# Performance work log

Measured on AMD Instinct MI355X. Metric: run time of the kernel, lower is better.

Reference implementation:

```python
import jax, jax.numpy as jnp
import numpy as np

RADIUS = 0.1
NSAMPLE = 32


def setup_inputs() -> dict:
    key = jax.random.key(0)
    k1, k2, k3, k4 = jax.random.split(key, 4)
    B, N, C = 8, 8192, 64
    C_in = 3 + C  # relative xyz concatenated with features
    H1, H2 = 64, 128
    xyz = jax.random.uniform(k1, (B, N, 3), dtype=jnp.float32)  # points in unit cube
    features = jax.random.normal(k2, (B, C, N), dtype=jnp.float32)
    W1 = jax.random.normal(k3, (H1, C_in), dtype=jnp.float32) / np.sqrt(C_in)
    b1 = jnp.zeros((H1,), dtype=jnp.float32)
    W2 = jax.random.normal(k4, (H2, H1), dtype=jnp.float32) / np.sqrt(H1)
    b2 = jnp.zeros((H2,), dtype=jnp.float32)
    return {"xyz": xyz, "features": features, "W1": W1, "b1": b1,
            "W2": W2, "b2": b2, "npoint": 2048}


def _ball_query(xyz, new_xyz, radius, nsample):
    # xyz: (B,N,3), new_xyz: (B,S,3) -> idx (B,S,nsample) int32
    N = xyz.shape[1]
    d2 = jnp.sum((new_xyz[:, :, None, :] - xyz[:, None, :, :]) ** 2, axis=-1)  # (B,S,N)
    mask = d2 < radius * radius
    # sort key: in-ball points keep their index (ascending order first),
    # out-of-ball points pushed behind by +N
    ar = jnp.arange(N, dtype=jnp.int32)
    key = jnp.where(mask, ar, ar + N)
    idx_sorted = jnp.argsort(key, axis=-1)[..., :nsample].astype(jnp.int32)  # (B,S,ns)
    count = jnp.sum(mask, axis=-1)  # (B,S)
    first = idx_sorted[..., :1]
    slot = jnp.arange(nsample)
    # CUDA ball_query pads missing slots with the first found index
    return jnp.where(slot[None, None, :] < count[..., None], idx_sorted, first)


def reference(xyz, features, W1, b1, W2, b2, npoint):
    # use_fps=False: sample_idxs = arange(npoint) -> new_xyz = first npoint points
    new_xyz = xyz[:, :npoint, :]  # (B,S,3)
    idx = _ball_query(xyz, new_xyz, RADIUS, NSAMPLE)  # (B,S,ns)

    # QueryAndGroup: gather xyz (centered) + features, concat on channel dim
    gx = jax.vmap(lambda p, i: p[i])(xyz, idx)  # (B,S,ns,3)
    rel = gx - new_xyz[:, :, None, :]  # (B,S,ns,3)
    gf = jax.vmap(lambda f, i: f[:, i])(features, idx)  # (B,C,S,ns)
    grouped = jnp.concatenate([jnp.transpose(rel, (0, 3, 1, 2)), gf], axis=1)  # (B,3+C,S,ns)

    # SharedMLP: 1x1 conv + ReLU stack
    h = jax.nn.relu(jnp.einsum('oc,bcsn->bosn', W1, grouped) + b1[None, :, None, None])
    h = jax.nn.relu(jnp.einsum('oc,bcsn->bosn', W2, h) + b2[None, :, None, None])

    # max_pool2d over nsample, squeeze
    new_features = jnp.max(h, axis=-1)  # (B,H2,S)
    return new_xyz, new_features
```

## Files before the change

### kernel.cpp

```cpp
#include <hip/hip_runtime.h>
#include <hip/hip_bf16.h>

#define B_      8
#define N_      8192
#define C_      64
#define H1_     64
#define H2_     128
#define NS      32
#define NPOINT  2048
#define NGROUP  (B_ * NPOINT)
#define NXYZ    (B_ * NPOINT * 3)
#define GD      10
#define NCP     1024

typedef short bf16x8 __attribute__((ext_vector_type(8)));
typedef short bf16x4 __attribute__((ext_vector_type(4)));
typedef float f32x4  __attribute__((ext_vector_type(4)));

#define MFMA32 __builtin_amdgcn_mfma_f32_16x16x32_bf16
#define MFMA16 __builtin_amdgcn_mfma_f32_16x16x16bf16_1k

__device__ inline unsigned short f2bf(float f) {
    unsigned u = __builtin_bit_cast(unsigned, f);
    return (unsigned short)((u + 0x7FFF + ((u >> 16) & 1)) >> 16);
}
__device__ inline float bf2f(unsigned short h) {
    unsigned u = ((unsigned)h) << 16;
    return __builtin_bit_cast(float, u);
}

__global__ __launch_bounds__(256) void prep_all_kernel(
    const float* __restrict__ xyz, const float* __restrict__ feat,
    const float* __restrict__ W1, const float* __restrict__ W2,
    unsigned short* __restrict__ fT_hi, unsigned short* __restrict__ fT_lo,
    int* __restrict__ cellStart, int* __restrict__ sortedId,
    float* __restrict__ sortedXyz,
    unsigned short* __restrict__ W1x_hi, unsigned short* __restrict__ W1x_lo,
    unsigned short* __restrict__ W2x_hi, unsigned short* __restrict__ W2x_lo,
    float* __restrict__ out)
{
    __shared__ char smem[64 * 65 * 4];
    int blk = blockIdx.x, t = threadIdx.x;

    if (blk < 1024) {
        float (*tile)[65] = reinterpret_cast<float(*)[65]>(smem);
        int b = blk >> 7, nt = blk & 127;
        int n0 = nt * 64;
        int tx = t & 63, ty = t >> 6;
#pragma unroll
        for (int k = 0; k < 16; ++k) {
            int c = ty * 16 + k;
            tile[c][tx] = feat[((size_t)b * C_ + c) * N_ + n0 + tx];
        }
        __syncthreads();
#pragma unroll
        for (int k = 0; k < 16; ++k) {
            int n = ty * 16 + k;
            float v = tile[tx][n];
            unsigned short h = f2bf(v);
            size_t dst = ((size_t)(b * N_ + n0 + n)) * C_ + tx;
            fT_hi[dst] = h;
            fT_lo[dst] = f2bf(v - bf2f(h));
        }
    } else if (blk < 1032) {
        int* hist = reinterpret_cast<int*>(smem);
        int* wsum = hist + NCP;
        int b = blk - 1024;
        for (int i = t; i < NCP; i += 256) hist[i] = 0;
        __syncthreads();
        const float* base = xyz + (size_t)b * N_ * 3;
        for (int k = 0; k < N_ / 256; ++k) {
            int i = k * 256 + t;
            float x = base[i * 3], y = base[i * 3 + 1], z = base[i * 3 + 2];
            int c = (((int)(x * 9.999f)) * GD + (int)(y * 9.999f)) * GD + (int)(z * 9.999f);
            atomicAdd(&hist[c], 1);
        }
        __syncthreads();
        int h0 = hist[t * 4], h1 = hist[t * 4 + 1], h2 = hist[t * 4 + 2], h3 = hist[t * 4 + 3];
        int s = h0 + h1 + h2 + h3;
        int lane = t & 63, w = t >> 6;
        int v = s;
        for (int d = 1; d < 64; d <<= 1) {
            int o = __shfl_up(v, d);
            if (lane >= d) v += o;
        }
        if (lane == 63) wsum[w] = v;
        __syncthreads();
        int wofs = 0;
        for (int i = 0; i < 4; ++i) wofs += (i < w) ? wsum[i] : 0;
        int excl = wofs + v - s;
        int* cs = cellStart + b * (NCP + 1);
        cs[t * 4]     = excl;
        cs[t * 4 + 1] = excl + h0;
        cs[t * 4 + 2] = excl + h0 + h1;
        cs[t * 4 + 3] = excl + h0 + h1 + h2;
        if (t == 255) cs[NCP] = excl + s;
        __syncthreads();
        hist[t * 4] = excl; hist[t * 4 + 1] = excl + h0;
        hist[t * 4 + 2] = excl + h0 + h1; hist[t * 4 + 3] = excl + h0 + h1 + h2;
        __syncthreads();
        for (int k = 0; k < N_ / 256; ++k) {
            int i = k * 256 + t;
            float x = base[i * 3], y = base[i * 3 + 1], z = base[i * 3 + 2];
            int c = (((int)(x * 9.999f)) * GD + (int)(y * 9.999f)) * GD + (int)(z * 9.999f);
            int pos = atomicAdd(&hist[c], 1);
            sortedId[b * N_ + pos] = i;
            float* d = sortedXyz + ((size_t)(b * N_) + pos) * 3;
            d[0] = x; d[1] = y; d[2] = z;
        }
    } else if (blk < 1056) {
        const float4* src = reinterpret_cast<const float4*>(xyz);
        float4* dst = reinterpret_cast<float4*>(out);
#pragma unroll
        for (int k = 0; k < 2; ++k) {
            int i4 = (blk - 1032) * 512 + k * 256 + t;
            int b = i4 / 1536, r = i4 - b * 1536;
            dst[i4] = src[b * 6144 + r];
        }
    } else {
        int tg = (blk - 1056) * 256 + t;
        if (tg < 6144) {
            int j = tg & 7, cl = (tg >> 3) & 15, kq = (tg >> 7) & 3, t2 = tg >> 9;
            int kt = t2 % 3, mt = t2 / 3;
            int row = mt * 16 + cl, k = kt * 32 + kq * 8 + j;
            float wv = 0.f;
            if (k < 64) wv = W1[row * 67 + 3 + k];
            else if (k < 67) wv = W1[row * 67 + (k - 64)];
            unsigned short h = f2bf(wv);
            W1x_hi[tg] = h; W1x_lo[tg] = f2bf(wv - bf2f(h));
        }
        if (tg < 8192) {
            int i = tg & 3, half = (tg >> 2) & 1, cl = (tg >> 3) & 15;
            int kq = (tg >> 7) & 3, kt2p = (tg >> 9) & 1, mt = tg >> 10;
            int row = mt * 16 + cl, k = kt2p * 32 + half * 16 + kq * 4 + i;
            float wv = W2[row * 64 + k];
            unsigned short h = f2bf(wv);
            W2x_hi[tg] = h; W2x_lo[tg] = f2bf(wv - bf2f(h));
        }
    }
}

__global__ __launch_bounds__(256) void fused_kernel(
    const float* __restrict__ xyz,
    const int* __restrict__ cellStart,
    const int* __restrict__ sortedId,
    const float* __restrict__ sortedXyz,
    const unsigned short* __restrict__ fT_hi, const unsigned short* __restrict__ fT_lo,
    const unsigned short* __restrict__ W1x_hi, const unsigned short* __restrict__ W1x_lo,
    const float* __restrict__ b1,
    const unsigned short* __restrict__ W2x_hi, const unsigned short* __restrict__ W2x_lo,
    const float* __restrict__ b2,
    float* __restrict__ out)
{
    __shared__ int shbuf[4][128];
    int t = threadIdx.x;
    int w = t >> 6, lane = t & 63;
    int g = blockIdx.x * 4 + w;
    int b = g >> 11, s = g & 2047;

    const float* qp = xyz + ((size_t)(b * N_) + s) * 3;
    float qx = qp[0], qy = qp[1], qz = qp[2];
    const float r2 = 0.01f;
    unsigned long long lmask = (1ull << lane) - 1ull;

    int cx = (int)(qx * 9.999f), cy = (int)(qy * 9.999f), cz = (int)(qz * 9.999f);
    int xlo = max(cx - 1, 0), xhi = min(cx + 1, GD - 1);
    int ylo = max(cy - 1, 0), yhi = min(cy + 1, GD - 1);
    int zlo = max(cz - 1, 0), zhi = min(cz + 1, GD - 1);
    int nx = xhi - xlo + 1, ny = yhi - ylo + 1;
    int nruns = nx * ny;

    const int* cs = cellStart + b * (NCP + 1);
    int start = 0, len = 0;
    if (lane < nruns) {
        int xi = xlo + lane / ny, yi = ylo + lane % ny;
        int cbase = (xi * GD + yi) * GD;
        start = cs[cbase + zlo];
        len = cs[cbase + zhi + 1] - start;
    }
    int v = len;
    for (int d = 1; d < 64; d <<= 1) {
        int o = __shfl_up(v, d);
        if (lane >= d) v += o;
    }
    int T = __shfl(v, 63);
    int excl = v - len;
    int ro[9], rs[9];
#pragma unroll
    for (int rr = 0; rr < 9; ++rr) {
        int oo = __shfl(excl, rr);
        int ss = __shfl(start, rr);
        bool live = rr < nruns;
        ro[rr] = live ? oo : 0x7fffffff;
        rs[rr] = live ? (ss - oo) : 0;
    }

    int cnt = 0;
    for (int k0 = 0; k0 < T; k0 += 64) {
        int pos = k0 + lane;
        bool valid = pos < T;
        int basev = rs[0];
#pragma unroll
        for (int rr = 1; rr < 9; ++rr)
            basev = (ro[rr] <= pos) ? rs[rr] : basev;
        float px = 1.e30f, py = 1.e30f, pz = 1.e30f;
        int pid = 0;
        if (valid) {
            int src = basev + pos;
            const float* pp = sortedXyz + ((size_t)(b * N_) + src) * 3;
            px = pp[0]; py = pp[1]; pz = pp[2];
            pid = sortedId[b * N_ + src];
        }
        float dx = __fsub_rn(px, qx);
        float dy = __fsub_rn(py, qy);
        float dz = __fsub_rn(pz, qz);
        float d2 = __fadd_rn(__fadd_rn(__fmul_rn(dx, dx), __fmul_rn(dy, dy)),
                             __fmul_rn(dz, dz));
        bool pred = valid && (d2 < r2);
        unsigned long long m = __ballot(pred);
        if (pred) {
            int p = cnt + __builtin_popcountll(m & lmask);
            if (p < 128) shbuf[w][p] = pid;
        }
        cnt += __builtin_popcountll(m);
    }

    const int INF = 0x7fffffff;
    int v0 = (lane < cnt && lane < 128) ? shbuf[w][lane] : INF;
    int v1 = (lane + 64 < cnt) ? shbuf[w][lane + 64] : INF;
#pragma unroll
    for (int k = 2; k <= 128; k <<= 1) {
#pragma unroll
        for (int j = 64; j >= 1; j >>= 1) {
            if (j > (k >> 1)) continue;
            if (j == 64) {
                int lo = min(v0, v1), hi = max(v0, v1);
                v0 = lo; v1 = hi;
            } else {
                int p0 = __shfl_xor(v0, j), p1 = __shfl_xor(v1, j);
                bool lower = (lane & j) == 0;
                bool asc0 = (lane & k) == 0;
                bool asc1 = ((lane + 64) & k) == 0;
                v0 = (lower == asc0) ? min(v0, p0) : max(v0, p0);
                v1 = (lower == asc1) ? min(v1, p1) : max(v1, p1);
            }
        }
    }
    int first = __shfl(v0, 0);
    int cl = lane & 15, kq = lane >> 4;
    int sv0 = __shfl(v0, cl);
    int sv1 = __shfl(v0, cl + 16);
    int i0 = (cl < cnt) ? sv0 : first;
    int i1 = (cl + 16 < cnt) ? sv1 : first;

    bf16x8 bh[2][2], bl[2][2];
#pragma unroll
    for (int nt = 0; nt < 2; ++nt) {
        int i = nt ? i1 : i0;
        size_t rowoff = ((size_t)(b * N_ + i)) * C_ + kq * 8;
#pragma unroll
        for (int kt = 0; kt < 2; ++kt) {
            bh[nt][kt] = *reinterpret_cast<const bf16x8*>(fT_hi + rowoff + kt * 32);
            bl[nt][kt] = *reinterpret_cast<const bf16x8*>(fT_lo + rowoff + kt * 32);
        }
    }
    bf16x8 brel[2];
#pragma unroll
    for (int nt = 0; nt < 2; ++nt) {
        int i = nt ? i1 : i0;
        bf16x8 vv = (bf16x8)(short)0;
        if (kq == 0) {
            const float* p = xyz + ((size_t)(b * N_) + i) * 3;
            vv[0] = (short)f2bf(__fsub_rn(p[0], qx));
            vv[1] = (short)f2bf(__fsub_rn(p[1], qy));
            vv[2] = (short)f2bf(__fsub_rn(p[2], qz));
        }
        brel[nt] = vv;
    }

    f32x4 acc[4][2];
#pragma unroll
    for (int mt = 0; mt < 4; ++mt) {
        f32x4 bias = *reinterpret_cast<const f32x4*>(b1 + mt * 16 + kq * 4);
        acc[mt][0] = bias;
        acc[mt][1] = bias;
    }
#pragma unroll
    for (int mt = 0; mt < 4; ++mt) {
        bf16x8 ah0 = *reinterpret_cast<const bf16x8*>(W1x_hi + (mt * 3 + 0) * 512 + lane * 8);
        bf16x8 ah1 = *reinterpret_cast<const bf16x8*>(W1x_hi + (mt * 3 + 1) * 512 + lane * 8);
        bf16x8 ah2 = *reinterpret_cast<const bf16x8*>(W1x_hi + (mt * 3 + 2) * 512 + lane * 8);
        bf16x8 al0 = *reinterpret_cast<const bf16x8*>(W1x_lo + (mt * 3 + 0) * 512 + lane * 8);
        bf16x8 al1 = *reinterpret_cast<const bf16x8*>(W1x_lo + (mt * 3 + 1) * 512 + lane * 8);
#pragma unroll
        for (int nt = 0; nt < 2; ++nt) {
            f32x4 a = acc[mt][nt];
            a = MFMA32(ah0, bh[nt][0], a, 0, 0, 0);
            a = MFMA32(ah0, bl[nt][0], a, 0, 0, 0);
            a = MFMA32(al0, bh[nt][0], a, 0, 0, 0);
            a = MFMA32(ah1, bh[nt][1], a, 0, 0, 0);
            a = MFMA32(ah1, bl[nt][1], a, 0, 0, 0);
            a = MFMA32(al1, bh[nt][1], a, 0, 0, 0);
            a = MFMA32(ah2, brel[nt], a, 0, 0, 0);
            acc[mt][nt] = a;
        }
    }

    bf16x4 p2h[4][2], p2l[4][2];
#pragma unroll
    for (int kt2 = 0; kt2 < 4; ++kt2)
#pragma unroll
        for (int nt = 0; nt < 2; ++nt) {
            f32x4 h = acc[kt2][nt];
            bf16x4 hh, hl;
#pragma unroll
            for (int i = 0; i < 4; ++i) {
                float hr = fmaxf(h[i], 0.f);
                unsigned short hb = f2bf(hr);
                hh[i] = (short)hb;
                hl[i] = (short)f2bf(hr - bf2f(hb));
            }
            p2h[kt2][nt] = hh;
            p2l[kt2][nt] = hl;
        }

    float* ys = reinterpret_cast<float*>(&shbuf[0][0]);
#pragma unroll
    for (int hm = 0; hm < 2; ++hm) {
        f32x4 acc2[4][2];
#pragma unroll
        for (int mt4 = 0; mt4 < 4; ++mt4) {
            f32x4 bias = *reinterpret_cast<const f32x4*>(b2 + (hm * 4 + mt4) * 16 + kq * 4);
            acc2[mt4][0] = bias;
            acc2[mt4][1] = bias;
        }
#pragma unroll
        for (int mt4 = 0; mt4 < 4; ++mt4) {
            int mt = hm * 4 + mt4;
#pragma unroll
            for (int kt2p = 0; kt2p < 2; ++kt2p) {
                bf16x8 ah = *reinterpret_cast<const bf16x8*>(W2x_hi + (mt * 2 + kt2p) * 512 + lane * 8);
                bf16x8 al = *reinterpret_cast<const bf16x8*>(W2x_lo + (mt * 2 + kt2p) * 512 + lane * 8);
                bf16x4 ah_a = __builtin_shufflevector(ah, ah, 0, 1, 2, 3);
                bf16x4 ah_b = __builtin_shufflevector(ah, ah, 4, 5, 6, 7);
                bf16x4 al_a = __builtin_shufflevector(al, al, 0, 1, 2, 3);
                bf16x4 al_b = __builtin_shufflevector(al, al, 4, 5, 6, 7);
#pragma unroll
                for (int nt = 0; nt < 2; ++nt) {
                    f32x4 a = acc2[mt4][nt];
                    a = MFMA16(ah_a, p2h[kt2p * 2][nt], a, 0, 0, 0);
                    a = MFMA16(ah_a, p2l[kt2p * 2][nt], a, 0, 0, 0);
                    a = MFMA16(al_a, p2h[kt2p * 2][nt], a, 0, 0, 0);
                    a = MFMA16(ah_b, p2h[kt2p * 2 + 1][nt], a, 0, 0, 0);
                    a = MFMA16(ah_b, p2l[kt2p * 2 + 1][nt], a, 0, 0, 0);
                    a = MFMA16(al_b, p2h[kt2p * 2 + 1][nt], a, 0, 0, 0);
                    acc2[mt4][nt] = a;
                }
            }
        }
#pragma unroll
        for (int mt4 = 0; mt4 < 4; ++mt4) {
            f32x4 m;
#pragma unroll
            for (int r = 0; r < 4; ++r)
                m[r] = fmaxf(fmaxf(acc2[mt4][0][r], 0.f), fmaxf(acc2[mt4][1][r], 0.f));
#pragma unroll
            for (int mask = 1; mask <= 8; mask <<= 1)
#pragma unroll
                for (int r = 0; r < 4; ++r)
                    m[r] = fmaxf(m[r], __shfl_xor(m[r], mask));
            if (cl == 0)
                *reinterpret_cast<f32x4*>(ys + w * 128 + (hm * 4 + mt4) * 16 + kq * 4) = m;
        }
    }

    __syncthreads();
    if (t < 128) {
        int o = t;
        int bb = blockIdx.x >> 9;
        int s0 = (blockIdx.x & 511) * 4;
        float4 vv = { ys[0 * 128 + o], ys[1 * 128 + o], ys[2 * 128 + o], ys[3 * 128 + o] };
        *reinterpret_cast<float4*>(out + NXYZ + ((size_t)(bb * H2_ + o)) * NPOINT + s0) = vv;
    }
}

extern "C" void kernel_launch(void* const* d_in, const int* in_sizes, int n_in,
                              void* d_out, int out_size, void* d_ws, size_t ws_size,
                              hipStream_t stream)
{
    const float* xyz  = (const float*)d_in[0];
    const float* feat = (const float*)d_in[1];
    const float* W1   = (const float*)d_in[2];
    const float* b1   = (const float*)d_in[3];
    const float* W2   = (const float*)d_in[4];
    const float* b2   = (const float*)d_in[5];
    float* out = (float*)d_out;

    char* ws = (char*)d_ws;
    size_t off = 0;
    unsigned short* W1x_hi = (unsigned short*)(ws + off);  off += 6144 * 2;
    unsigned short* W1x_lo = (unsigned short*)(ws + off);  off += 6144 * 2;
    unsigned short* W2x_hi = (unsigned short*)(ws + off);  off += 8192 * 2;
    unsigned short* W2x_lo = (unsigned short*)(ws + off);  off += 8192 * 2;
    off = (off + 255) & ~(size_t)255;
    int* cellStart = (int*)(ws + off);                     off += (size_t)B_ * (NCP + 1) * 4;
    int* sortedId = (int*)(ws + off);                      off += (size_t)B_ * N_ * 4;
    float* sortedXyz = (float*)(ws + off);                 off += (size_t)B_ * N_ * 3 * 4;
    off = (off + 255) & ~(size_t)255;
    unsigned short* fT_hi = (unsigned short*)(ws + off);   off += (size_t)B_ * N_ * C_ * 2;
    unsigned short* fT_lo = (unsigned short*)(ws + off);   off += (size_t)B_ * N_ * C_ * 2;

    prep_all_kernel<<<1088, 256, 0, stream>>>(
        xyz, feat, W1, W2, fT_hi, fT_lo, cellStart, sortedId, sortedXyz,
        W1x_hi, W1x_lo, W2x_hi, W2x_lo, out);
    fused_kernel<<<NGROUP / 4, 256, 0, stream>>>(
        xyz, cellStart, sortedId, sortedXyz, fT_hi, fT_lo,
        W1x_hi, W1x_lo, b1, W2x_hi, W2x_lo, b2, out);
}
```

Measured before the change: 178.3 us.

## Use 16x16x32 MFMA for layer 2 via permuted W1 rows; split grid build

```diff
diff --git a/kernel.cpp b/kernel.cpp
--- a/kernel.cpp
+++ b/kernel.cpp
@@ -14,36 +14,87 @@
 #define NCP     1024
 
 typedef short bf16x8 __attribute__((ext_vector_type(8)));
-typedef short bf16x4 __attribute__((ext_vector_type(4)));
 typedef float f32x4  __attribute__((ext_vector_type(4)));
 
 #define MFMA32 __builtin_amdgcn_mfma_f32_16x16x32_bf16
-#define MFMA16 __builtin_amdgcn_mfma_f32_16x16x16bf16_1k
 
 __device__ inline unsigned short f2bf(float f) {
-    unsigned u = __builtin_bit_cast(unsigned, f);
-    return (unsigned short)((u + 0x7FFF + ((u >> 16) & 1)) >> 16);
+    __hip_bfloat16 h = __float2bfloat16(f);
+    return __builtin_bit_cast(unsigned short, h);
 }
 __device__ inline float bf2f(unsigned short h) {
     unsigned u = ((unsigned)h) << 16;
     return __builtin_bit_cast(float, u);
+}
+
+__device__ __host__ inline int permrow(int p) {
+    int mt = p >> 4, rho = p & 15;
+    return ((mt >> 1) << 5) + ((rho >> 2) << 3) + ((mt & 1) << 2) + (rho & 3);
+}
+
+__global__ __launch_bounds__(1024) void grid_kernel(
+    const float* __restrict__ xyz,
+    int* __restrict__ cellStart,
+    int* __restrict__ sortedId,
+    float* __restrict__ sortedXyz)
+{
+    __shared__ int hist[NCP];
+    __shared__ int wsum[16];
+    int b = blockIdx.x, t = threadIdx.x;
+    hist[t] = 0;
+    __syncthreads();
+    const float* base = xyz + (size_t)b * N_ * 3;
+#pragma unroll
+    for (int k = 0; k < N_ / 1024; ++k) {
+        int i = k * 1024 + t;
+        float x = base[i * 3], y = base[i * 3 + 1], z = base[i * 3 + 2];
+        int c = (((int)(x * 9.999f)) * GD + (int)(y * 9.999f)) * GD + (int)(z * 9.999f);
+        atomicAdd(&hist[c], 1);
+    }
+    __syncthreads();
+    int s = hist[t];
+    int lane = t & 63, w = t >> 6;
+    int v = s;
+    for (int d = 1; d < 64; d <<= 1) {
+        int o = __shfl_up(v, d);
+        if (lane >= d) v += o;
+    }
+    if (lane == 63) wsum[w] = v;
+    __syncthreads();
+    int wofs = 0;
+#pragma unroll
+    for (int i = 0; i < 16; ++i) wofs += (i < w) ? wsum[i] : 0;
+    int excl = wofs + v - s;
+    int* cs = cellStart + b * (NCP + 1);
+    cs[t] = excl;
+    if (t == 1023) cs[NCP] = excl + s;
+    __syncthreads();
+    hist[t] = excl;
+    __syncthreads();
+#pragma unroll
+    for (int k = 0; k < N_ / 1024; ++k) {
+        int i = k * 1024 + t;
+        float x = base[i * 3], y = base[i * 3 + 1], z = base[i * 3 + 2];
+        int c = (((int)(x * 9.999f)) * GD + (int)(y * 9.999f)) * GD + (int)(z * 9.999f);
+        int pos = atomicAdd(&hist[c], 1);
+        sortedId[b * N_ + pos] = i;
+        float* d = sortedXyz + ((size_t)(b * N_) + pos) * 3;
+        d[0] = x; d[1] = y; d[2] = z;
+    }
 }
 
 __global__ __launch_bounds__(256) void prep_all_kernel(
     const float* __restrict__ xyz, const float* __restrict__ feat,
     const float* __restrict__ W1, const float* __restrict__ W2,
     unsigned short* __restrict__ fT_hi, unsigned short* __restrict__ fT_lo,
-    int* __restrict__ cellStart, int* __restrict__ sortedId,
-    float* __restrict__ sortedXyz,
     unsigned short* __restrict__ W1x_hi, unsigned short* __restrict__ W1x_lo,
     unsigned short* __restrict__ W2x_hi, unsigned short* __restrict__ W2x_lo,
     float* __restrict__ out)
 {
-    __shared__ char smem[64 * 65 * 4];
+    __shared__ float tile[64][65];
     int blk = blockIdx.x, t = threadIdx.x;
 
     if (blk < 1024) {
-        float (*tile)[65] = reinterpret_cast<float(*)[65]>(smem);
         int b = blk >> 7, nt = blk & 127;
         int n0 = nt * 64;
         int tx = t & 63, ty = t >> 6;
@@ -62,67 +113,22 @@
             fT_hi[dst] = h;
             fT_lo[dst] = f2bf(v - bf2f(h));
         }
-    } else if (blk < 1032) {
-        int* hist = reinterpret_cast<int*>(smem);
-        int* wsum = hist + NCP;
-        int b = blk - 1024;
-        for (int i = t; i < NCP; i += 256) hist[i] = 0;
-        __syncthreads();
-        const float* base = xyz + (size_t)b * N_ * 3;
-        for (int k = 0; k < N_ / 256; ++k) {
-            int i = k * 256 + t;
-            float x = base[i * 3], y = base[i * 3 + 1], z = base[i * 3 + 2];
-            int c = (((int)(x * 9.999f)) * GD + (int)(y * 9.999f)) * GD + (int)(z * 9.999f);
-            atomicAdd(&hist[c], 1);
-        }
-        __syncthreads();
-        int h0 = hist[t * 4], h1 = hist[t * 4 + 1], h2 = hist[t * 4 + 2], h3 = hist[t * 4 + 3];
-        int s = h0 + h1 + h2 + h3;
-        int lane = t & 63, w = t >> 6;
-        int v = s;
-        for (int d = 1; d < 64; d <<= 1) {
-            int o = __shfl_up(v, d);
-            if (lane >= d) v += o;
-        }
-        if (lane == 63) wsum[w] = v;
-        __syncthreads();
-        int wofs = 0;
-        for (int i = 0; i < 4; ++i) wofs += (i < w) ? wsum[i] : 0;
-        int excl = wofs + v - s;
-        int* cs = cellStart + b * (NCP + 1);
-        cs[t * 4]     = excl;
-        cs[t * 4 + 1] = excl + h0;
-        cs[t * 4 + 2] = excl + h0 + h1;
-        cs[t * 4 + 3] = excl + h0 + h1 + h2;
-        if (t == 255) cs[NCP] = excl + s;
-        __syncthreads();
-        hist[t * 4] = excl; hist[t * 4 + 1] = excl + h0;
-        hist[t * 4 + 2] = excl + h0 + h1; hist[t * 4 + 3] = excl + h0 + h1 + h2;
-        __syncthreads();
-        for (int k = 0; k < N_ / 256; ++k) {
-            int i = k * 256 + t;
-            float x = base[i * 3], y = base[i * 3 + 1], z = base[i * 3 + 2];
-            int c = (((int)(x * 9.999f)) * GD + (int)(y * 9.999f)) * GD + (int)(z * 9.999f);
-            int pos = atomicAdd(&hist[c], 1);
-            sortedId[b * N_ + pos] = i;
-            float* d = sortedXyz + ((size_t)(b * N_) + pos) * 3;
-            d[0] = x; d[1] = y; d[2] = z;
-        }
-    } else if (blk < 1056) {
+    } else if (blk < 1048) {
         const float4* src = reinterpret_cast<const float4*>(xyz);
         float4* dst = reinterpret_cast<float4*>(out);
 #pragma unroll
         for (int k = 0; k < 2; ++k) {
-            int i4 = (blk - 1032) * 512 + k * 256 + t;
+            int i4 = (blk - 1024) * 512 + k * 256 + t;
             int b = i4 / 1536, r = i4 - b * 1536;
             dst[i4] = src[b * 6144 + r];
         }
     } else {
-        int tg = (blk - 1056) * 256 + t;
+        int tg = (blk - 1048) * 256 + t;
         if (tg < 6144) {
             int j = tg & 7, cl = (tg >> 3) & 15, kq = (tg >> 7) & 3, t2 = tg >> 9;
             int kt = t2 % 3, mt = t2 / 3;
-            int row = mt * 16 + cl, k = kt * 32 + kq * 8 + j;
+            int row = permrow(mt * 16 + cl);
+            int k = kt * 32 + kq * 8 + j;
             float wv = 0.f;
             if (k < 64) wv = W1[row * 67 + 3 + k];
             else if (k < 67) wv = W1[row * 67 + (k - 64)];
@@ -130,9 +136,9 @@
             W1x_hi[tg] = h; W1x_lo[tg] = f2bf(wv - bf2f(h));
         }
         if (tg < 8192) {
-            int i = tg & 3, half = (tg >> 2) & 1, cl = (tg >> 3) & 15;
-            int kq = (tg >> 7) & 3, kt2p = (tg >> 9) & 1, mt = tg >> 10;
-            int row = mt * 16 + cl, k = kt2p * 32 + half * 16 + kq * 4 + i;
+            int j = tg & 7, cl = (tg >> 3) & 15, kq = (tg >> 7) & 3;
+            int kt = (tg >> 9) & 1, mt2 = tg >> 10;
+            int row = mt2 * 16 + cl, k = kt * 32 + kq * 8 + j;
             float wv = W2[row * 64 + k];
             unsigned short h = f2bf(wv);
             W2x_hi[tg] = h; W2x_lo[tg] = f2bf(wv - bf2f(h));
@@ -281,7 +287,8 @@
     f32x4 acc[4][2];
 #pragma unroll
     for (int mt = 0; mt < 4; ++mt) {
-        f32x4 bias = *reinterpret_cast<const f32x4*>(b1 + mt * 16 + kq * 4);
+        int bn = ((mt >> 1) << 5) + kq * 8 + ((mt & 1) << 2);
+        f32x4 bias = *reinterpret_cast<const f32x4*>(b1 + bn);
         acc[mt][0] = bias;
         acc[mt][1] = bias;
     }
@@ -306,22 +313,24 @@
         }
     }
 
-    bf16x4 p2h[4][2], p2l[4][2];
-#pragma unroll
-    for (int kt2 = 0; kt2 < 4; ++kt2)
+    bf16x8 p2h[2][2], p2l[2][2];
+#pragma unroll
+    for (int kt = 0; kt < 2; ++kt)
 #pragma unroll
         for (int nt = 0; nt < 2; ++nt) {
-            f32x4 h = acc[kt2][nt];
-            bf16x4 hh, hl;
+            bf16x8 hh, hl;
 #pragma unroll
             for (int i = 0; i < 4; ++i) {
-                float hr = fmaxf(h[i], 0.f);
-                unsigned short hb = f2bf(hr);
-                hh[i] = (short)hb;
-                hl[i] = (short)f2bf(hr - bf2f(hb));
+                float va = fmaxf(acc[kt * 2 + 0][nt][i], 0.f);
+                float vb = fmaxf(acc[kt * 2 + 1][nt][i], 0.f);
+                unsigned short ha = f2bf(va), hb = f2bf(vb);
+                hh[i]     = (short)ha;
+                hh[4 + i] = (short)hb;
+                hl[i]     = (short)f2bf(va - bf2f(ha));
+                hl[4 + i] = (short)f2bf(vb - bf2f(hb));
             }
-            p2h[kt2][nt] = hh;
-            p2l[kt2][nt] = hl;
+            p2h[kt][nt] = hh;
+            p2l[kt][nt] = hl;
         }
 
     float* ys = reinterpret_cast<float*>(&shbuf[0][0]);
@@ -336,24 +345,17 @@
         }
 #pragma unroll
         for (int mt4 = 0; mt4 < 4; ++mt4) {
-            int mt = hm * 4 + mt4;
-#pragma unroll
-            for (int kt2p = 0; kt2p < 2; ++kt2p) {
-                bf16x8 ah = *reinterpret_cast<const bf16x8*>(W2x_hi + (mt * 2 + kt2p) * 512 + lane * 8);
-                bf16x8 al = *reinterpret_cast<const bf16x8*>(W2x_lo + (mt * 2 + kt2p) * 512 + lane * 8);
-                bf16x4 ah_a = __builtin_shufflevector(ah, ah, 0, 1, 2, 3);
-                bf16x4 ah_b = __builtin_shufflevector(ah, ah, 4, 5, 6, 7);
-                bf16x4 al_a = __builtin_shufflevector(al, al, 0, 1, 2, 3);
-                bf16x4 al_b = __builtin_shufflevector(al, al, 4, 5, 6, 7);
+            int mt2 = hm * 4 + mt4;
+#pragma unroll
+            for (int kt = 0; kt < 2; ++kt) {
+                bf16x8 ah = *reinterpret_cast<const bf16x8*>(W2x_hi + (mt2 * 2 + kt) * 512 + lane * 8);
+                bf16x8 al = *reinterpret_cast<const bf16x8*>(W2x_lo + (mt2 * 2 + kt) * 512 + lane * 8);
 #pragma unroll
                 for (int nt = 0; nt < 2; ++nt) {
                     f32x4 a = acc2[mt4][nt];
-                    a = MFMA16(ah_a, p2h[kt2p * 2][nt], a, 0, 0, 0);
-                    a = MFMA16(ah_a, p2l[kt2p * 2][nt], a, 0, 0, 0);
-                    a = MFMA16(al_a, p2h[kt2p * 2][nt], a, 0, 0, 0);
-                    a = MFMA16(ah_b, p2h[kt2p * 2 + 1][nt], a, 0, 0, 0);
-                    a = MFMA16(ah_b, p2l[kt2p * 2 + 1][nt], a, 0, 0, 0);
-                    a = MFMA16(al_b, p2h[kt2p * 2 + 1][nt], a, 0, 0, 0);
+                    a = MFMA32(ah, p2h[kt][nt], a, 0, 0, 0);
+                    a = MFMA32(ah, p2l[kt][nt], a, 0, 0, 0);
+                    a = MFMA32(al, p2h[kt][nt], a, 0, 0, 0);
                     acc2[mt4][nt] = a;
                 }
             }
@@ -410,9 +412,9 @@
     unsigned short* fT_hi = (unsigned short*)(ws + off);   off += (size_t)B_ * N_ * C_ * 2;
     unsigned short* fT_lo = (unsigned short*)(ws + off);   off += (size_t)B_ * N_ * C_ * 2;
 
-    prep_all_kernel<<<1088, 256, 0, stream>>>(
-        xyz, feat, W1, W2, fT_hi, fT_lo, cellStart, sortedId, sortedXyz,
-        W1x_hi, W1x_lo, W2x_hi, W2x_lo, out);
+    grid_kernel<<<B_, 1024, 0, stream>>>(xyz, cellStart, sortedId, sortedXyz);
+    prep_all_kernel<<<1080, 256, 0, stream>>>(
+        xyz, feat, W1, W2, fT_hi, fT_lo, W1x_hi, W1x_lo, W2x_hi, W2x_lo, out);
     fused_kernel<<<NGROUP / 4, 256, 0, stream>>>(
         xyz, cellStart, sortedId, sortedXyz, fT_hi, fT_lo,
         W1x_hi, W1x_lo, b1, W2x_hi, W2x_lo, b2, out);
```

Result: faster. 169.4 us (-5.0%).
